# Kernel tuning notes

Hardware: AMD Instinct MI355X
Metric: run time of the kernel (lower is better)

## Reference

```python
import jax, jax.numpy as jnp
import numpy as np

N = 100000

def gcn_conv(x, src, dst, W, b, n):
    # x: [N, Fin]; src/dst: [E'] (self-loops already included); W: [Fin, Fout]
    h = x @ W  # [N, Fout]
    deg = jax.ops.segment_sum(jnp.ones_like(dst, dtype=h.dtype), dst, num_segments=n)  # [N]
    dinv = deg ** -0.5  # deg >= 1 due to self-loops
    norm = dinv[src] * dinv[dst]  # [E']
    msg = h[src] * norm[:, None]  # gather + scale, [E', Fout]
    out = jax.ops.segment_sum(msg, dst, num_segments=n)  # scatter-add to targets
    return out + b

def setup_inputs() -> dict:
    key = jax.random.key(0)
    k1, k2, k3, k4, k5, k6 = jax.random.split(key, 6)
    x = jax.random.normal(k1, (N, 128), dtype=jnp.float32)
    edge_index = jax.random.randint(k2, (2, 1600000), 0, N, dtype=jnp.int32)
    W1 = jax.random.normal(k3, (128, 64), dtype=jnp.float32) * 0.1
    b1 = jnp.zeros((64,), dtype=jnp.float32)
    W2 = jax.random.normal(k4, (64, 41), dtype=jnp.float32) * 0.1
    b2 = jnp.zeros((41,), dtype=jnp.float32)
    return {"x": x, "edge_index": edge_index, "W1": W1, "b1": b1, "W2": W2, "b2": b2}

def reference(x, edge_index, W1, b1, W2, b2):
    n = x.shape[0]
    loops = jnp.arange(n, dtype=edge_index.dtype)
    src = jnp.concatenate([edge_index[0], loops])  # add self-loops (PyG gcn_norm default)
    dst = jnp.concatenate([edge_index[1], loops])
    # dropout is identity in eval mode (self.training=False)
    h = gcn_conv(x, src, dst, W1, b1, n)
    h = jax.nn.relu(h)
    out = gcn_conv(h, src, dst, W2, b2, n)
    return out
```

## Files before the change

kernel.cpp:

```cpp
#include <hip/hip_runtime.h>


#define FIN 128
#define F1  64
#define F2  41
#define F2P 48

#define BSH    8
#define BCAP   6144
#define NBMAX  512
#define CHUNK  4096

#define MT 128
#define KC 16

__device__ __forceinline__ unsigned short f2bf(float f) {
    unsigned u = __builtin_bit_cast(unsigned, f);
    u += 0x7FFFu + ((u >> 16) & 1u);
    return (unsigned short)(u >> 16);
}
__device__ __forceinline__ float bf2f(unsigned short h) {
    unsigned u = ((unsigned)h) << 16;
    return __builtin_bit_cast(float, u);
}

__global__ __launch_bounds__(256) void k_part(
    const int* __restrict__ src, const int* __restrict__ dst,
    int* __restrict__ gcur, int* __restrict__ pairs, int E) {
    __shared__ int hist[NBMAX];
    int tid = threadIdx.x;
    int e0  = blockIdx.x * CHUNK;
    int ds[CHUNK / 256], ss[CHUNK / 256];
#pragma unroll
    for (int j = 0; j < CHUNK / 256; j++) {
        int e = e0 + j * 256 + tid;
        if (e < E) { ds[j] = dst[e]; ss[j] = src[e]; } else ds[j] = -1;
    }
    for (int i = tid; i < NBMAX; i += 256) hist[i] = 0;
    __syncthreads();
#pragma unroll
    for (int j = 0; j < CHUNK / 256; j++)
        if (ds[j] >= 0) atomicAdd(&hist[ds[j] >> BSH], 1);
    __syncthreads();
    for (int i = tid; i < NBMAX; i += 256) {
        int c = hist[i];
        hist[i] = c ? atomicAdd(&gcur[i], c) : 0;
    }
    __syncthreads();
#pragma unroll
    for (int j = 0; j < CHUNK / 256; j++) {
        if (ds[j] >= 0) {
            int b = ds[j] >> BSH;
            int pos = atomicAdd(&hist[b], 1);
            if (pos < BCAP) pairs[b * BCAP + pos] = (ss[j] << BSH) | (ds[j] & 255);
        }
    }
}

__global__ __launch_bounds__(NBMAX) void k_bucketbase(
    const int* __restrict__ gcur, int* __restrict__ bbase,
    int* __restrict__ rowptr, int nbuck, int n, int E) {
    __shared__ int s[NBMAX];
    int t = threadIdx.x;
    int v = (t < nbuck) ? gcur[t] : 0;
    s[t] = v;
    __syncthreads();
    for (int off = 1; off < NBMAX; off <<= 1) {
        int val = s[t];
        int add = (t >= off) ? s[t - off] : 0;
        __syncthreads();
        s[t] = val + add;
        __syncthreads();
    }
    if (t < nbuck) bbase[t] = s[t] - v;
    if (t == 0) rowptr[n] = E;
}

__global__ __launch_bounds__(256) void k_build(
    const int* __restrict__ gcur, const int* __restrict__ bbase,
    const int* __restrict__ pairs, int* __restrict__ adj,
    int* __restrict__ rowptr, float* __restrict__ dinv, int n) {
    __shared__ int lcnt[256];
    __shared__ int lex[256];
    __shared__ int lcur[256];
    __shared__ int ladj[BCAP];
    int tid = threadIdx.x;
    int b   = blockIdx.x;
    int base  = bbase[b];
    int cntb  = gcur[b]; if (cntb > BCAP) cntb = BCAP;
    int node0 = b << BSH;
    const int* pb = pairs + (size_t)b * BCAP;

    lcnt[tid] = 0;
    __syncthreads();
    for (int k = tid; k < cntb; k += 256) atomicAdd(&lcnt[pb[k] & 255], 1);
    __syncthreads();
    int own = lcnt[tid];
    lex[tid] = own;
    __syncthreads();
    for (int off = 1; off < 256; off <<= 1) {
        int val = lex[tid];
        int add = (tid >= off) ? lex[tid - off] : 0;
        __syncthreads();
        lex[tid] = val + add;
        __syncthreads();
    }
    int excl = lex[tid] - own;
    __syncthreads();
    lex[tid]  = excl;
    lcur[tid] = excl;
    __syncthreads();
    for (int k = tid; k < cntb; k += 256) {
        int pk  = pb[k];
        int pos = atomicAdd(&lcur[pk & 255], 1);
        ladj[pos] = pk >> BSH;
    }
    __syncthreads();
    for (int k = tid; k < cntb; k += 256) adj[base + k] = ladj[k];
    int node = node0 + tid;
    if (node < n) {
        rowptr[node] = base + lex[tid];
        dinv[node]   = rsqrtf((float)own + 1.0f);
    }
}

__global__ __launch_bounds__(256) void k_mm1(
    const float* __restrict__ x, const float* __restrict__ W1,
    const float* __restrict__ dinv, unsigned short* __restrict__ hs, int n) {
    __shared__ float Ws[FIN * F1];
    __shared__ float As[KC][MT];
    int t  = threadIdx.x;
    int n0 = blockIdx.x * MT;
#pragma unroll
    for (int j = 0; j < 8; j++) {
        int f = j * 256 + t;
        ((float4*)Ws)[f] = ((const float4*)W1)[f];
    }
    int m0 = (t & 15) * 8;
    int c0 = (t >> 4) * 4;
    int m_l = t & 127;
    int kh  = (t >> 7) * 8;
    bool mvalid = (n0 + m_l) < n;
    const float* xrow = x + (size_t)(n0 + m_l) * FIN + kh;
    float acc[8][4] = {};
    for (int kc = 0; kc < FIN; kc += KC) {
        __syncthreads();
        float4 v0 = mvalid ? *(const float4*)(xrow + kc)     : float4{0.f,0.f,0.f,0.f};
        float4 v1 = mvalid ? *(const float4*)(xrow + kc + 4) : float4{0.f,0.f,0.f,0.f};
        As[kh + 0][m_l] = v0.x; As[kh + 1][m_l] = v0.y;
        As[kh + 2][m_l] = v0.z; As[kh + 3][m_l] = v0.w;
        As[kh + 4][m_l] = v1.x; As[kh + 5][m_l] = v1.y;
        As[kh + 6][m_l] = v1.z; As[kh + 7][m_l] = v1.w;
        __syncthreads();
#pragma unroll
        for (int k = 0; k < KC; k++) {
            float4 a0 = *(const float4*)&As[k][m0];
            float4 a1 = *(const float4*)&As[k][m0 + 4];
            float4 w  = *(const float4*)&Ws[(kc + k) * F1 + c0];
            float a[8] = {a0.x, a0.y, a0.z, a0.w, a1.x, a1.y, a1.z, a1.w};
#pragma unroll
            for (int i = 0; i < 8; i++) {
                acc[i][0] += a[i] * w.x;
                acc[i][1] += a[i] * w.y;
                acc[i][2] += a[i] * w.z;
                acc[i][3] += a[i] * w.w;
            }
        }
    }
#pragma unroll
    for (int i = 0; i < 8; i++) {
        int node = n0 + m0 + i;
        if (node < n) {
            float dv = dinv[node];
            ushort4 o = { f2bf(acc[i][0] * dv), f2bf(acc[i][1] * dv),
                          f2bf(acc[i][2] * dv), f2bf(acc[i][3] * dv) };
            *(ushort4*)&hs[(size_t)node * F1 + c0] = o;
        }
    }
}

__global__ __launch_bounds__(256) void k_agg1(
    const int* __restrict__ rowptr, const int* __restrict__ adj,
    const unsigned short* __restrict__ hs, const float* __restrict__ dinv,
    const float* __restrict__ b1, float* __restrict__ h1, int n) {
    int node = blockIdx.x * 4 + (threadIdx.x >> 6);
    if (node >= n) return;
    int lane = threadIdx.x & 63;
    int beg = rowptr[node], end = rowptr[node + 1];
    float acc = bf2f(hs[(size_t)node * F1 + lane]);
    int i = beg;
    for (; i + 4 <= end; i += 4) {
        int s0 = adj[i], s1 = adj[i + 1], s2 = adj[i + 2], s3 = adj[i + 3];
        float a0 = bf2f(hs[(size_t)s0 * F1 + lane]);
        float a1 = bf2f(hs[(size_t)s1 * F1 + lane]);
        float a2 = bf2f(hs[(size_t)s2 * F1 + lane]);
        float a3 = bf2f(hs[(size_t)s3 * F1 + lane]);
        acc += a0 + a1 + a2 + a3;
    }
    for (; i < end; i++) acc += bf2f(hs[(size_t)adj[i] * F1 + lane]);
    float v = acc * dinv[node] + b1[lane];
    h1[(size_t)node * F1 + lane] = v > 0.f ? v : 0.f;
}

__global__ __launch_bounds__(256) void k_mm2(
    const float* __restrict__ h1, const float* __restrict__ W2,
    const float* __restrict__ dinv, unsigned short* __restrict__ hs2, int n) {
    __shared__ float Ws[F1 * F2P];
    __shared__ float As[KC][MT];
    int t  = threadIdx.x;
    int n0 = blockIdx.x * MT;
    for (int idx = t; idx < F1 * F2P; idx += 256) {
        int k = idx / F2P, c = idx - k * F2P;
        Ws[idx] = (c < F2) ? W2[k * F2 + c] : 0.f;
    }
    int m0 = (t & 15) * 8;
    int c0 = (t >> 4) * 4;
    bool compute = (t < 192);
    int m_l = t & 127;
    int kh  = (t >> 7) * 8;
    bool mvalid = (n0 + m_l) < n;
    const float* hrow = h1 + (size_t)(n0 + m_l) * F1 + kh;
    float acc[8][4] = {};
    for (int kc = 0; kc < F1; kc += KC) {
        __syncthreads();
        float4 v0 = mvalid ? *(const float4*)(hrow + kc)     : float4{0.f,0.f,0.f,0.f};
        float4 v1 = mvalid ? *(const float4*)(hrow + kc + 4) : float4{0.f,0.f,0.f,0.f};
        As[kh + 0][m_l] = v0.x; As[kh + 1][m_l] = v0.y;
        As[kh + 2][m_l] = v0.z; As[kh + 3][m_l] = v0.w;
        As[kh + 4][m_l] = v1.x; As[kh + 5][m_l] = v1.y;
        As[kh + 6][m_l] = v1.z; As[kh + 7][m_l] = v1.w;
        __syncthreads();
        if (compute) {
#pragma unroll
            for (int k = 0; k < KC; k++) {
                float4 a0 = *(const float4*)&As[k][m0];
                float4 a1 = *(const float4*)&As[k][m0 + 4];
                float4 w  = *(const float4*)&Ws[(kc + k) * F2P + c0];
                float a[8] = {a0.x, a0.y, a0.z, a0.w, a1.x, a1.y, a1.z, a1.w};
#pragma unroll
                for (int i = 0; i < 8; i++) {
                    acc[i][0] += a[i] * w.x;
                    acc[i][1] += a[i] * w.y;
                    acc[i][2] += a[i] * w.z;
                    acc[i][3] += a[i] * w.w;
                }
            }
        }
    }
    if (compute) {
#pragma unroll
        for (int i = 0; i < 8; i++) {
            int node = n0 + m0 + i;
            if (node < n) {
                float dv = dinv[node];
                ushort4 o = { f2bf(acc[i][0] * dv), f2bf(acc[i][1] * dv),
                              f2bf(acc[i][2] * dv), f2bf(acc[i][3] * dv) };
                *(ushort4*)&hs2[(size_t)node * F2P + c0] = o;
            }
        }
    }
}

__global__ __launch_bounds__(256) void k_agg2(
    const int* __restrict__ rowptr, const int* __restrict__ adj,
    const unsigned short* __restrict__ hs2, const float* __restrict__ dinv,
    const float* __restrict__ b2, float* __restrict__ out, int n) {
    int node = blockIdx.x * 4 + (threadIdx.x >> 6);
    if (node >= n) return;
    int lane = threadIdx.x & 63;
    int beg = rowptr[node], end = rowptr[node + 1];
    float acc = (lane < F2) ? bf2f(hs2[(size_t)node * F2P + lane]) : 0.f;
    int i = beg;
    for (; i + 4 <= end; i += 4) {
        int s0 = adj[i], s1 = adj[i + 1], s2 = adj[i + 2], s3 = adj[i + 3];
        if (lane < F2) {
            acc += bf2f(hs2[(size_t)s0 * F2P + lane]);
            acc += bf2f(hs2[(size_t)s1 * F2P + lane]);
            acc += bf2f(hs2[(size_t)s2 * F2P + lane]);
            acc += bf2f(hs2[(size_t)s3 * F2P + lane]);
        }
    }
    for (; i < end; i++)
        if (lane < F2) acc += bf2f(hs2[(size_t)adj[i] * F2P + lane]);
    if (lane < F2) out[(size_t)node * F2 + lane] = acc * dinv[node] + b2[lane];
}

__global__ void k_zero(int* __restrict__ p, int n) {
    int i = blockIdx.x * blockDim.x + threadIdx.x;
    if (i < n) p[i] = 0;
}

extern "C" void kernel_launch(void* const* d_in, const int* in_sizes, int n_in,
                              void* d_out, int out_size, void* d_ws, size_t ws_size,
                              hipStream_t stream) {
    const float* x  = (const float*)d_in[0];
    const int*   ei = (const int*)d_in[1];
    const float* W1 = (const float*)d_in[2];
    const float* b1 = (const float*)d_in[3];
    const float* W2 = (const float*)d_in[4];
    const float* b2 = (const float*)d_in[5];
    float* out = (float*)d_out;

    const int n = in_sizes[0] / FIN;
    const int E = in_sizes[1] / 2;
    const int* src = ei;
    const int* dst = ei + E;
    const int nbuck   = (n + 255) >> BSH;
    const int nchunks = (E + CHUNK - 1) / CHUNK;
    const int nmm     = (n + MT - 1) / MT;

    char* ws = (char*)d_ws;
    size_t off = 0;
    auto alloc = [&](size_t bytes) {
        void* p = ws + off;
        off = (off + bytes + 511) & ~(size_t)511;
        return p;
    };
    int*   gcur   = (int*)alloc((size_t)NBMAX * 4);
    int*   bbase  = (int*)alloc((size_t)NBMAX * 4);
    int*   pairs  = (int*)alloc((size_t)nbuck * BCAP * 4);
    int*   adj    = (int*)alloc((size_t)E * 4);
    int*   rowptr = (int*)alloc((size_t)(n + 1) * 4);
    float* dinv   = (float*)alloc((size_t)n * 4);
    unsigned short* bufHS = (unsigned short*)alloc((size_t)n * F1 * 2);
    float* bufH1  = (float*)alloc((size_t)n * F1 * 4);

    k_zero<<<(NBMAX + 255) / 256, 256, 0, stream>>>(gcur, NBMAX);
    k_part<<<nchunks, 256, 0, stream>>>(src, dst, gcur, pairs, E);
    k_bucketbase<<<1, NBMAX, 0, stream>>>(gcur, bbase, rowptr, nbuck, n, E);
    k_build<<<nbuck, 256, 0, stream>>>(gcur, bbase, pairs, adj, rowptr, dinv, n);

    k_mm1<<<nmm, 256, 0, stream>>>(x, W1, dinv, bufHS, n);
    k_agg1<<<(n + 3) / 4, 256, 0, stream>>>(rowptr, adj, bufHS, dinv, b1, bufH1, n);

    k_mm2<<<nmm, 256, 0, stream>>>(bufH1, W2, dinv, bufHS, n);
    k_agg2<<<(n + 3) / 4, 256, 0, stream>>>(rowptr, adj, bufHS, dinv, b2, out, n);
}
```

Measured before the change: 322.0 us.

## Fuse layer-1 aggregation with second matmul and restructure CSR build

The edge partition kernel now stages each chunk in shared memory and writes it to the bucket array in sorted order, so global stores are coalesced. The separate bucket-base scan kernel is dropped: each build block claims its adjacency offset with an atomic, and row start plus degree are stored together as an int2. Layer-1 aggregation is fused with the 64x41 matmul using wave shuffles and W2 held in shared memory, so the fp32 h1 intermediate and one launch disappear. Both aggregation kernels load neighbour indices cooperatively and issue 16 gathers at once for more memory-level parallelism. In exchange the adjacency order is now nondeterministic, and the fused per-node matmul does 64 shuffles per node plus much larger shared-memory use in the partition kernel.

```diff
diff --git a/kernel.cpp b/kernel.cpp
--- a/kernel.cpp
+++ b/kernel.cpp
@@ -9,7 +9,7 @@
 #define BSH    8
 #define BCAP   6144
 #define NBMAX  512
-#define CHUNK  4096
+#define CHUNK_P 8192
 
 #define MT 128
 #define KC 16
@@ -24,73 +24,83 @@
     return __builtin_bit_cast(float, u);
 }
 
+__global__ void k_zero(int* __restrict__ p, int n) {
+    int i = blockIdx.x * blockDim.x + threadIdx.x;
+    if (i < n) p[i] = 0;
+}
+
 __global__ __launch_bounds__(256) void k_part(
     const int* __restrict__ src, const int* __restrict__ dst,
     int* __restrict__ gcur, int* __restrict__ pairs, int E) {
     __shared__ int hist[NBMAX];
+    __shared__ int gsh[NBMAX];
+    __shared__ int lex[256];
+    __shared__ int limg[CHUNK_P];
+    __shared__ int lsh[CHUNK_P];
+    __shared__ int stot;
     int tid = threadIdx.x;
-    int e0  = blockIdx.x * CHUNK;
-    int ds[CHUNK / 256], ss[CHUNK / 256];
-#pragma unroll
-    for (int j = 0; j < CHUNK / 256; j++) {
+    int e0  = blockIdx.x * CHUNK_P;
+    hist[tid] = 0; hist[tid + 256] = 0;
+    __syncthreads();
+    for (int j = 0; j < CHUNK_P / 256; j++) {
         int e = e0 + j * 256 + tid;
-        if (e < E) { ds[j] = dst[e]; ss[j] = src[e]; } else ds[j] = -1;
-    }
-    for (int i = tid; i < NBMAX; i += 256) hist[i] = 0;
-    __syncthreads();
-#pragma unroll
-    for (int j = 0; j < CHUNK / 256; j++)
-        if (ds[j] >= 0) atomicAdd(&hist[ds[j] >> BSH], 1);
-    __syncthreads();
-    for (int i = tid; i < NBMAX; i += 256) {
-        int c = hist[i];
-        hist[i] = c ? atomicAdd(&gcur[i], c) : 0;
-    }
-    __syncthreads();
-#pragma unroll
-    for (int j = 0; j < CHUNK / 256; j++) {
-        if (ds[j] >= 0) {
-            int b = ds[j] >> BSH;
-            int pos = atomicAdd(&hist[b], 1);
-            if (pos < BCAP) pairs[b * BCAP + pos] = (ss[j] << BSH) | (ds[j] & 255);
-        }
-    }
-}
-
-__global__ __launch_bounds__(NBMAX) void k_bucketbase(
-    const int* __restrict__ gcur, int* __restrict__ bbase,
-    int* __restrict__ rowptr, int nbuck, int n, int E) {
-    __shared__ int s[NBMAX];
-    int t = threadIdx.x;
-    int v = (t < nbuck) ? gcur[t] : 0;
-    s[t] = v;
-    __syncthreads();
-    for (int off = 1; off < NBMAX; off <<= 1) {
-        int val = s[t];
-        int add = (t >= off) ? s[t - off] : 0;
-        __syncthreads();
-        s[t] = val + add;
-        __syncthreads();
-    }
-    if (t < nbuck) bbase[t] = s[t] - v;
-    if (t == 0) rowptr[n] = E;
+        if (e < E) atomicAdd(&hist[dst[e] >> BSH], 1);
+    }
+    __syncthreads();
+    int b0 = 2 * tid, b1 = 2 * tid + 1;
+    int c0 = hist[b0], c1 = hist[b1];
+    int s  = c0 + c1;
+    lex[tid] = s;
+    __syncthreads();
+    for (int off = 1; off < 256; off <<= 1) {
+        int v = lex[tid];
+        int a = (tid >= off) ? lex[tid - off] : 0;
+        __syncthreads();
+        lex[tid] = v + a;
+        __syncthreads();
+    }
+    int incl = lex[tid];
+    if (tid == 255) stot = incl;
+    int ex = incl - s;
+    int l0 = ex, l1 = ex + c0;
+    int g0 = c0 ? atomicAdd(&gcur[b0], c0) : 0;
+    int g1 = c1 ? atomicAdd(&gcur[b1], c1) : 0;
+    hist[b0] = l0; hist[b1] = l1;
+    gsh[b0]  = b0 * BCAP + g0 - l0;
+    gsh[b1]  = b1 * BCAP + g1 - l1;
+    __syncthreads();
+    for (int j = 0; j < CHUNK_P / 256; j++) {
+        int e = e0 + j * 256 + tid;
+        if (e < E) {
+            int d = dst[e], sv = src[e];
+            int b = d >> BSH;
+            int p = atomicAdd(&hist[b], 1);
+            limg[p] = (sv << BSH) | (d & 255);
+            lsh[p]  = gsh[b];
+        }
+    }
+    __syncthreads();
+    int tot = stot;
+    for (int k = tid; k < tot; k += 256)
+        pairs[k + lsh[k]] = limg[k];
 }
 
 __global__ __launch_bounds__(256) void k_build(
-    const int* __restrict__ gcur, const int* __restrict__ bbase,
-    const int* __restrict__ pairs, int* __restrict__ adj,
-    int* __restrict__ rowptr, float* __restrict__ dinv, int n) {
+    const int* __restrict__ gcur, const int* __restrict__ pairs,
+    int* __restrict__ adjcur, int* __restrict__ adj,
+    int2* __restrict__ rowinfo, float* __restrict__ dinv, int n) {
     __shared__ int lcnt[256];
     __shared__ int lex[256];
     __shared__ int lcur[256];
     __shared__ int ladj[BCAP];
+    __shared__ int sbase;
     int tid = threadIdx.x;
     int b   = blockIdx.x;
-    int base  = bbase[b];
     int cntb  = gcur[b]; if (cntb > BCAP) cntb = BCAP;
     int node0 = b << BSH;
     const int* pb = pairs + (size_t)b * BCAP;
 
+    if (tid == 0) sbase = atomicAdd(adjcur, cntb);
     lcnt[tid] = 0;
     __syncthreads();
     for (int k = tid; k < cntb; k += 256) atomicAdd(&lcnt[pb[k] & 255], 1);
@@ -116,11 +126,12 @@
         ladj[pos] = pk >> BSH;
     }
     __syncthreads();
+    int base = sbase;
     for (int k = tid; k < cntb; k += 256) adj[base + k] = ladj[k];
     int node = node0 + tid;
     if (node < n) {
-        rowptr[node] = base + lex[tid];
-        dinv[node]   = rsqrtf((float)own + 1.0f);
+        rowinfo[node] = make_int2(base + lex[tid], own);
+        dinv[node]    = rsqrtf((float)own + 1.0f);
     }
 }
 
@@ -179,115 +190,101 @@
     }
 }
 
-__global__ __launch_bounds__(256) void k_agg1(
-    const int* __restrict__ rowptr, const int* __restrict__ adj,
+__global__ __launch_bounds__(256) void k_agg1mm2(
+    const int2* __restrict__ rowinfo, const int* __restrict__ adj,
     const unsigned short* __restrict__ hs, const float* __restrict__ dinv,
-    const float* __restrict__ b1, float* __restrict__ h1, int n) {
+    const float* __restrict__ b1, const float* __restrict__ W2,
+    unsigned short* __restrict__ hs2, int n, int E) {
+    __shared__ float W2s[F1 * F2P];
+    int tid = threadIdx.x;
+    for (int idx = tid; idx < F1 * F2P; idx += 256) {
+        int k = idx / F2P, c = idx - k * F2P;
+        W2s[idx] = (c < F2) ? W2[k * F2 + c] : 0.f;
+    }
+    __syncthreads();
+    int node = blockIdx.x * 4 + (tid >> 6);
+    if (node >= n) return;
+    int lane = tid & 63;
+    int2 ri = rowinfo[node];
+    int beg = ri.x, deg = ri.y;
+    float dv = dinv[node];
+    const unsigned short* hsl = hs + lane;
+    float acc = bf2f(hsl[(size_t)node * F1]);
+    for (int base = 0; base < deg; base += 64) {
+        int m = deg - base; if (m > 64) m = 64;
+        int idx2 = beg + base + lane;
+        int myoff = adj[idx2 < E ? idx2 : 0] << 6;
+        int e = 0;
+        for (; e + 16 <= m; e += 16) {
+            int o[16]; float a[16];
+#pragma unroll
+            for (int q = 0; q < 16; q++) o[q] = __shfl(myoff, e + q);
+#pragma unroll
+            for (int q = 0; q < 16; q++) a[q] = bf2f(hsl[(size_t)o[q]]);
+            float s1 = ((a[0]+a[1])+(a[2]+a[3])) + ((a[4]+a[5])+(a[6]+a[7]));
+            float s2 = ((a[8]+a[9])+(a[10]+a[11])) + ((a[12]+a[13])+(a[14]+a[15]));
+            acc += s1 + s2;
+        }
+        for (; e + 4 <= m; e += 4) {
+            int o0 = __shfl(myoff, e), o1 = __shfl(myoff, e + 1);
+            int o2 = __shfl(myoff, e + 2), o3 = __shfl(myoff, e + 3);
+            float a0 = bf2f(hsl[(size_t)o0]);
+            float a1 = bf2f(hsl[(size_t)o1]);
+            float a2 = bf2f(hsl[(size_t)o2]);
+            float a3 = bf2f(hsl[(size_t)o3]);
+            acc += (a0 + a1) + (a2 + a3);
+        }
+        for (; e < m; e++) acc += bf2f(hsl[(size_t)__shfl(myoff, e)]);
+    }
+    float v = acc * dv + b1[lane];
+    v = v > 0.f ? v : 0.f;
+    int c = (lane < F2P) ? lane : 0;
+    float o = 0.f;
+#pragma unroll
+    for (int k = 0; k < F1; k++)
+        o += __shfl(v, k) * W2s[k * F2P + c];
+    if (lane < F2P) hs2[(size_t)node * F2P + lane] = f2bf(o * dv);
+}
+
+__global__ __launch_bounds__(256) void k_agg2(
+    const int2* __restrict__ rowinfo, const int* __restrict__ adj,
+    const unsigned short* __restrict__ hs2, const float* __restrict__ dinv,
+    const float* __restrict__ b2, float* __restrict__ out, int n, int E) {
     int node = blockIdx.x * 4 + (threadIdx.x >> 6);
     if (node >= n) return;
     int lane = threadIdx.x & 63;
-    int beg = rowptr[node], end = rowptr[node + 1];
-    float acc = bf2f(hs[(size_t)node * F1 + lane]);
-    int i = beg;
-    for (; i + 4 <= end; i += 4) {
-        int s0 = adj[i], s1 = adj[i + 1], s2 = adj[i + 2], s3 = adj[i + 3];
-        float a0 = bf2f(hs[(size_t)s0 * F1 + lane]);
-        float a1 = bf2f(hs[(size_t)s1 * F1 + lane]);
-        float a2 = bf2f(hs[(size_t)s2 * F1 + lane]);
-        float a3 = bf2f(hs[(size_t)s3 * F1 + lane]);
-        acc += a0 + a1 + a2 + a3;
-    }
-    for (; i < end; i++) acc += bf2f(hs[(size_t)adj[i] * F1 + lane]);
-    float v = acc * dinv[node] + b1[lane];
-    h1[(size_t)node * F1 + lane] = v > 0.f ? v : 0.f;
-}
-
-__global__ __launch_bounds__(256) void k_mm2(
-    const float* __restrict__ h1, const float* __restrict__ W2,
-    const float* __restrict__ dinv, unsigned short* __restrict__ hs2, int n) {
-    __shared__ float Ws[F1 * F2P];
-    __shared__ float As[KC][MT];
-    int t  = threadIdx.x;
-    int n0 = blockIdx.x * MT;
-    for (int idx = t; idx < F1 * F2P; idx += 256) {
-        int k = idx / F2P, c = idx - k * F2P;
-        Ws[idx] = (c < F2) ? W2[k * F2 + c] : 0.f;
-    }
-    int m0 = (t & 15) * 8;
-    int c0 = (t >> 4) * 4;
-    bool compute = (t < 192);
-    int m_l = t & 127;
-    int kh  = (t >> 7) * 8;
-    bool mvalid = (n0 + m_l) < n;
-    const float* hrow = h1 + (size_t)(n0 + m_l) * F1 + kh;
-    float acc[8][4] = {};
-    for (int kc = 0; kc < F1; kc += KC) {
-        __syncthreads();
-        float4 v0 = mvalid ? *(const float4*)(hrow + kc)     : float4{0.f,0.f,0.f,0.f};
-        float4 v1 = mvalid ? *(const float4*)(hrow + kc + 4) : float4{0.f,0.f,0.f,0.f};
-        As[kh + 0][m_l] = v0.x; As[kh + 1][m_l] = v0.y;
-        As[kh + 2][m_l] = v0.z; As[kh + 3][m_l] = v0.w;
-        As[kh + 4][m_l] = v1.x; As[kh + 5][m_l] = v1.y;
-        As[kh + 6][m_l] = v1.z; As[kh + 7][m_l] = v1.w;
-        __syncthreads();
-        if (compute) {
-#pragma unroll
-            for (int k = 0; k < KC; k++) {
-                float4 a0 = *(const float4*)&As[k][m0];
-                float4 a1 = *(const float4*)&As[k][m0 + 4];
-                float4 w  = *(const float4*)&Ws[(kc + k) * F2P + c0];
-                float a[8] = {a0.x, a0.y, a0.z, a0.w, a1.x, a1.y, a1.z, a1.w};
-#pragma unroll
-                for (int i = 0; i < 8; i++) {
-                    acc[i][0] += a[i] * w.x;
-                    acc[i][1] += a[i] * w.y;
-                    acc[i][2] += a[i] * w.z;
-                    acc[i][3] += a[i] * w.w;
-                }
-            }
-        }
-    }
-    if (compute) {
-#pragma unroll
-        for (int i = 0; i < 8; i++) {
-            int node = n0 + m0 + i;
-            if (node < n) {
-                float dv = dinv[node];
-                ushort4 o = { f2bf(acc[i][0] * dv), f2bf(acc[i][1] * dv),
-                              f2bf(acc[i][2] * dv), f2bf(acc[i][3] * dv) };
-                *(ushort4*)&hs2[(size_t)node * F2P + c0] = o;
-            }
-        }
-    }
-}
-
-__global__ __launch_bounds__(256) void k_agg2(
-    const int* __restrict__ rowptr, const int* __restrict__ adj,
-    const unsigned short* __restrict__ hs2, const float* __restrict__ dinv,
-    const float* __restrict__ b2, float* __restrict__ out, int n) {
-    int node = blockIdx.x * 4 + (threadIdx.x >> 6);
-    if (node >= n) return;
-    int lane = threadIdx.x & 63;
-    int beg = rowptr[node], end = rowptr[node + 1];
-    float acc = (lane < F2) ? bf2f(hs2[(size_t)node * F2P + lane]) : 0.f;
-    int i = beg;
-    for (; i + 4 <= end; i += 4) {
-        int s0 = adj[i], s1 = adj[i + 1], s2 = adj[i + 2], s3 = adj[i + 3];
-        if (lane < F2) {
-            acc += bf2f(hs2[(size_t)s0 * F2P + lane]);
-            acc += bf2f(hs2[(size_t)s1 * F2P + lane]);
-            acc += bf2f(hs2[(size_t)s2 * F2P + lane]);
-            acc += bf2f(hs2[(size_t)s3 * F2P + lane]);
-        }
-    }
-    for (; i < end; i++)
-        if (lane < F2) acc += bf2f(hs2[(size_t)adj[i] * F2P + lane]);
+    int fl   = (lane < F2) ? lane : 0;
+    int2 ri = rowinfo[node];
+    int beg = ri.x, deg = ri.y;
+    const unsigned short* hsl = hs2 + fl;
+    float acc = bf2f(hsl[(size_t)node * F2P]);
+    for (int base = 0; base < deg; base += 64) {
+        int m = deg - base; if (m > 64) m = 64;
+        int idx2 = beg + base + lane;
+        int myoff = adj[idx2 < E ? idx2 : 0] * F2P;
+        int e = 0;
+        for (; e + 16 <= m; e += 16) {
+            int o[16]; float a[16];
+#pragma unroll
+            for (int q = 0; q < 16; q++) o[q] = __shfl(myoff, e + q);
+#pragma unroll
+            for (int q = 0; q < 16; q++) a[q] = bf2f(hsl[(size_t)o[q]]);
+            float s1 = ((a[0]+a[1])+(a[2]+a[3])) + ((a[4]+a[5])+(a[6]+a[7]));
+            float s2 = ((a[8]+a[9])+(a[10]+a[11])) + ((a[12]+a[13])+(a[14]+a[15]));
+            acc += s1 + s2;
+        }
+        for (; e + 4 <= m; e += 4) {
+            int o0 = __shfl(myoff, e), o1 = __shfl(myoff, e + 1);
+            int o2 = __shfl(myoff, e + 2), o3 = __shfl(myoff, e + 3);
+            float a0 = bf2f(hsl[(size_t)o0]);
+            float a1 = bf2f(hsl[(size_t)o1]);
+            float a2 = bf2f(hsl[(size_t)o2]);
+            float a3 = bf2f(hsl[(size_t)o3]);
+            acc += (a0 + a1) + (a2 + a3);
+        }
+        for (; e < m; e++) acc += bf2f(hsl[(size_t)__shfl(myoff, e)]);
+    }
     if (lane < F2) out[(size_t)node * F2 + lane] = acc * dinv[node] + b2[lane];
-}
-
-__global__ void k_zero(int* __restrict__ p, int n) {
-    int i = blockIdx.x * blockDim.x + threadIdx.x;
-    if (i < n) p[i] = 0;
 }
 
 extern "C" void kernel_launch(void* const* d_in, const int* in_sizes, int n_in,
@@ -306,8 +303,9 @@
     const int* src = ei;
     const int* dst = ei + E;
     const int nbuck   = (n + 255) >> BSH;
-    const int nchunks = (E + CHUNK - 1) / CHUNK;
+    const int nchunks = (E + CHUNK_P - 1) / CHUNK_P;
     const int nmm     = (n + MT - 1) / MT;
+    const int nagg    = (n + 3) / 4;
 
     char* ws = (char*)d_ws;
     size_t off = 0;
@@ -316,23 +314,18 @@
         off = (off + bytes + 511) & ~(size_t)511;
         return p;
     };
-    int*   gcur   = (int*)alloc((size_t)NBMAX * 4);
-    int*   bbase  = (int*)alloc((size_t)NBMAX * 4);
-    int*   pairs  = (int*)alloc((size_t)nbuck * BCAP * 4);
-    int*   adj    = (int*)alloc((size_t)E * 4);
-    int*   rowptr = (int*)alloc((size_t)(n + 1) * 4);
-    float* dinv   = (float*)alloc((size_t)n * 4);
-    unsigned short* bufHS = (unsigned short*)alloc((size_t)n * F1 * 2);
-    float* bufH1  = (float*)alloc((size_t)n * F1 * 4);
-
-    k_zero<<<(NBMAX + 255) / 256, 256, 0, stream>>>(gcur, NBMAX);
+    int*   gcur    = (int*)alloc((size_t)(NBMAX + 1) * 4);
+    int*   pairs   = (int*)alloc((size_t)nbuck * BCAP * 4);
+    int*   adj     = (int*)alloc((size_t)E * 4);
+    int2*  rowinfo = (int2*)alloc((size_t)n * 8);
+    float* dinv    = (float*)alloc((size_t)n * 4);
+    unsigned short* hs1 = (unsigned short*)alloc((size_t)n * F1 * 2);
+    unsigned short* hs2 = (unsigned short*)alloc((size_t)n * F2P * 2);
+
+    k_zero<<<(NBMAX + 256) / 256, 256, 0, stream>>>(gcur, NBMAX + 1);
     k_part<<<nchunks, 256, 0, stream>>>(src, dst, gcur, pairs, E);
-    k_bucketbase<<<1, NBMAX, 0, stream>>>(gcur, bbase, rowptr, nbuck, n, E);
-    k_build<<<nbuck, 256, 0, stream>>>(gcur, bbase, pairs, adj, rowptr, dinv, n);
-
-    k_mm1<<<nmm, 256, 0, stream>>>(x, W1, dinv, bufHS, n);
-    k_agg1<<<(n + 3) / 4, 256, 0, stream>>>(rowptr, adj, bufHS, dinv, b1, bufH1, n);
-
-    k_mm2<<<nmm, 256, 0, stream>>>(bufH1, W2, dinv, bufHS, n);
-    k_agg2<<<(n + 3) / 4, 256, 0, stream>>>(rowptr, adj, bufHS, dinv, b2, out, n);
-}
+    k_build<<<nbuck, 256, 0, stream>>>(gcur, pairs, gcur + NBMAX, adj, rowinfo, dinv, n);
+    k_mm1<<<nmm, 256, 0, stream>>>(x, W1, dinv, hs1, n);
+    k_agg1mm2<<<nagg, 256, 0, stream>>>(rowinfo, adj, hs1, dinv, b1, W2, hs2, n, E);
+    k_agg2<<<nagg, 256, 0, stream>>>(rowinfo, adj, hs2, dinv, b2, out, n, E);
+}
```

New measurement: 370.8 us. 15.2% more time.
